# Optimization experiments

Hardware: AMD Instinct MI355X
Metric: run time of the kernel (lower is better)

The kernel has to match this reference:

```python
import jax, jax.numpy as jnp
import numpy as np

FACTOR = 1  # init factor -> top_k = int(factor * log(L))


def setup_inputs() -> dict:
    key = jax.random.key(0)
    kq, kk, kv = jax.random.split(key, 3)
    B, L, H, E = 16, 2048, 8, 64
    shape = (B, L, H, E)
    return {
        "queries": jax.random.normal(kq, shape, dtype=jnp.float32),
        "keys": jax.random.normal(kk, shape, dtype=jnp.float32),
        "values": jax.random.normal(kv, shape, dtype=jnp.float32),
    }


def reference(queries, keys, values):
    B, L, H, E = queries.shape
    # seq lens equal -> torch's pad/truncate branch is a no-op slice
    q = jnp.transpose(queries, (0, 2, 3, 1))  # [B,H,E,L]
    k = jnp.transpose(keys, (0, 2, 3, 1))
    v = jnp.transpose(values, (0, 2, 3, 1))

    # FFT-based circular cross-correlation along time
    qf = jnp.fft.rfft(q, axis=-1)
    kf = jnp.fft.rfft(k, axis=-1)
    corr = jnp.fft.irfft(qf * jnp.conj(kf), n=L, axis=-1)  # [B,H,E,L]

    top_k = int(FACTOR * np.log(L))  # static: 7 for L=2048
    mean_value = corr.mean(axis=(1, 2))  # mean over head then variates -> [B,L]
    # global (batch-averaged) top-k delays, shared across batch (training path)
    _, topk_index = jax.lax.top_k(mean_value.mean(axis=0), top_k)  # [k]
    # per-batch weights at those delays, softmax over k
    w = jax.nn.softmax(mean_value[:, topk_index], axis=-1)  # [B,k]

    # torch.roll(v, -d, -1)[..., t] == v[..., (t + d) % L]
    idx = (jnp.arange(L)[None, :] + topk_index[:, None]) % L  # [k,L]
    gathered = v[..., idx]  # [B,H,E,k,L]
    agg = jnp.einsum('bhekl,bk->bhel', gathered, w)  # weighted delay aggregation

    return jnp.transpose(agg, (0, 3, 1, 2))  # back to [B,L,H,E]
```

## Files before the change

kernel.cpp:

```cpp
#include <hip/hip_runtime.h>
#include <hip/hip_bf16.h>
#include <hip/hip_fp16.h>
#include <math.h>


#define B_ 16
#define L_ 2048
#define H_ 8
#define E_ 64
#define K_ 7
#define RS_ 2178

#define Z_OFF    0ull
#define PART_OFF 67108864ull
#define MV_OFF   (PART_OFF + 16777216ull)
#define TK_OFF   (MV_OFF + 131072ull)
#define W_OFF    (TK_OFF + 64ull)

__device__ __forceinline__ float2 cadd(float2 a, float2 b) { return make_float2(a.x + b.x, a.y + b.y); }
__device__ __forceinline__ float2 csub(float2 a, float2 b) { return make_float2(a.x - b.x, a.y - b.y); }
__device__ __forceinline__ float2 cmul(float2 a, float2 b) {
  return make_float2(fmaf(a.x, b.x, -a.y * b.y), fmaf(a.x, b.y, a.y * b.x));
}
__device__ __forceinline__ float2 cis(float ang) { float s, c; sincosf(ang, &s, &c); return make_float2(c, s); }

template<int S> __device__ __forceinline__ float2 rot90(float2 z) {
  return (S < 0) ? make_float2(z.y, -z.x) : make_float2(-z.y, z.x);
}
template<int S> __device__ __forceinline__ void dft4(float2& a, float2& b, float2& c, float2& d) {
  float2 t0 = cadd(a, c), t1 = csub(a, c), t2 = cadd(b, d), t3 = rot90<S>(csub(b, d));
  a = cadd(t0, t2); c = csub(t0, t2); b = cadd(t1, t3); d = csub(t1, t3);
}
template<int S> __device__ __forceinline__ void dft8(float2 v[8]) {
  const float RT = 0.70710678118654752f;
  const float SR = (S < 0) ? -RT : RT;
  float2 a0 = cadd(v[0], v[4]), a1 = cadd(v[1], v[5]), a2 = cadd(v[2], v[6]), a3 = cadd(v[3], v[7]);
  float2 b0 = csub(v[0], v[4]), b1 = csub(v[1], v[5]), b2 = csub(v[2], v[6]), b3 = csub(v[3], v[7]);
  b1 = cmul(b1, make_float2(RT, SR));
  b2 = rot90<S>(b2);
  b3 = cmul(b3, make_float2(-RT, SR));
  dft4<S>(a0, a1, a2, a3);
  dft4<S>(b0, b1, b2, b3);
  v[0] = a0; v[2] = a1; v[4] = a2; v[6] = a3;
  v[1] = b0; v[3] = b1; v[5] = b2; v[7] = b3;
}
__device__ __forceinline__ int sg(int e) { return e + (e >> 4); }

__device__ __forceinline__ float2 ld16(const __half2* p) { return __half22float2(*p); }
__device__ __forceinline__ void st16(__half2* p, float2 v) { *p = __float22half2_rn(v); }

__global__ __launch_bounds__(512) void pack_kernel(
    const float* __restrict__ q, const float* __restrict__ k,
    float4* __restrict__ z) {
  extern __shared__ float4 tile[];
  int tid = threadIdx.x;
  int l = blockIdx.x;
  int tl = l & 63, b = l >> 6;
  size_t rowbase = ((size_t)b * L_ + tl * 32) * 512;
  const float4* q4 = (const float4*)(q + rowbase);
  const float4* k4 = (const float4*)(k + rowbase);
#pragma unroll
  for (int pass = 0; pass < 8; ++pass) {
    int m = pass * 512 + tid;
    int j = m >> 7, cq = m & 127;
    float4 qv = q4[j * 128 + cq];
    float4 kv = k4[j * 128 + cq];
    float4 pk;
    ((__half2*)&pk)[0] = __float22half2_rn(make_float2(qv.x, kv.x));
    ((__half2*)&pk)[1] = __float22half2_rn(make_float2(qv.y, kv.y));
    ((__half2*)&pk)[2] = __float22half2_rn(make_float2(qv.z, kv.z));
    ((__half2*)&pk)[3] = __float22half2_rn(make_float2(qv.w, kv.w));
    tile[cq * 33 + j] = pk;
  }
  __syncthreads();
  float4* slab = z + (size_t)l * 4096;
#pragma unroll
  for (int pass = 0; pass < 8; ++pass) {
    int m = pass * 512 + tid;
    int cq = m >> 5, j = m & 31;
    slab[cq * 32 + j] = tile[cq * 33 + j];
  }
}

__global__ __launch_bounds__(512) void fft_corr_kernel(
    const float4* __restrict__ z, float2* __restrict__ part) {
  extern __shared__ __half2 dbuf[];
  int tid = threadIdx.x;
  int t = tid & 255;
  int half = tid >> 8;
  int j2 = t & 31, j3 = t & 3;
  int l = blockIdx.x;
  int cg = l & 63, b = l >> 6;
  int cq0 = cg * 2;
  const float4* zb = z + (size_t)b * 64 * 4096;

#pragma unroll
  for (int it = 0; it < 8; ++it) {
    int m = it * 512 + tid;
    int tl = m >> 6, inner = m & 63;
    int cqr = inner >> 5, j = inner & 31;
    float4 pk = zb[(size_t)tl * 4096 + (cq0 + cqr) * 32 + j];
    int sp = sg(tl * 32 + j);
    const __half2* hp = (const __half2*)&pk;
    dbuf[(cqr * 4 + 0) * RS_ + sp] = hp[0];
    dbuf[(cqr * 4 + 1) * RS_ + sp] = hp[1];
    dbuf[(cqr * 4 + 2) * RS_ + sp] = hp[2];
    dbuf[(cqr * 4 + 3) * RS_ + sp] = hp[3];
  }
  __syncthreads();

  float2 tw1[7], tw2[7], tw3[7];
  {
    float2 w1 = cis(-6.283185307179586f * (float)t  / 2048.0f);
    float2 w2 = cis(-6.283185307179586f * (float)j2 / 256.0f);
    float2 w3 = cis(-6.283185307179586f * (float)j3 / 32.0f);
    tw1[0] = w1; tw2[0] = w2; tw3[0] = w3;
#pragma unroll
    for (int kk = 1; kk < 7; ++kk) {
      tw1[kk] = cmul(tw1[kk - 1], w1);
      tw2[kk] = cmul(tw2[kk - 1], w2);
      tw3[kk] = cmul(tw3[kk - 1], w3);
    }
  }
  int base2 = (t >> 5) * 256 + j2;
  int base3 = (t >> 2) * 32 + j3;
  float2 acc[8];
#pragma unroll
  for (int kk = 0; kk < 8; ++kk) acc[kk] = make_float2(0.f, 0.f);

  for (int p = 0; p < 2; ++p) {
    __half2* A  = dbuf + (size_t)(4 * p + 2 * half) * RS_;
    __half2* Bf = A + RS_;
    float2 va[8], vb[8];
#pragma unroll
    for (int m = 0; m < 8; ++m) { va[m] = ld16(&A[sg(t + 256 * m)]); vb[m] = ld16(&Bf[sg(t + 256 * m)]); }
    dft8<-1>(va); dft8<-1>(vb);
#pragma unroll
    for (int kk = 1; kk < 8; ++kk) { va[kk] = cmul(va[kk], tw1[kk - 1]); vb[kk] = cmul(vb[kk], tw1[kk - 1]); }
#pragma unroll
    for (int kk = 0; kk < 8; ++kk) { st16(&A[sg(t + 256 * kk)], va[kk]); st16(&Bf[sg(t + 256 * kk)], vb[kk]); }
    __syncthreads();
#pragma unroll
    for (int m = 0; m < 8; ++m) { va[m] = ld16(&A[sg(base2 + 32 * m)]); vb[m] = ld16(&Bf[sg(base2 + 32 * m)]); }
    dft8<-1>(va); dft8<-1>(vb);
#pragma unroll
    for (int kk = 1; kk < 8; ++kk) { va[kk] = cmul(va[kk], tw2[kk - 1]); vb[kk] = cmul(vb[kk], tw2[kk - 1]); }
#pragma unroll
    for (int kk = 0; kk < 8; ++kk) { st16(&A[sg(base2 + 32 * kk)], va[kk]); st16(&Bf[sg(base2 + 32 * kk)], vb[kk]); }
    __syncthreads();
#pragma unroll
    for (int m = 0; m < 8; ++m) { va[m] = ld16(&A[sg(base3 + 4 * m)]); vb[m] = ld16(&Bf[sg(base3 + 4 * m)]); }
    dft8<-1>(va); dft8<-1>(vb);
#pragma unroll
    for (int kk = 1; kk < 8; ++kk) { va[kk] = cmul(va[kk], tw3[kk - 1]); vb[kk] = cmul(vb[kk], tw3[kk - 1]); }
#pragma unroll
    for (int kk = 0; kk < 8; ++kk) { st16(&A[sg(base3 + 4 * kk)], va[kk]); st16(&Bf[sg(base3 + 4 * kk)], vb[kk]); }
    __syncthreads();
#pragma unroll
    for (int kk = 0; kk < 8; ++kk) { va[kk] = ld16(&A[sg(8 * t + kk)]); vb[kk] = ld16(&Bf[sg(8 * t + kk)]); }
    dft4<-1>(va[0], va[1], va[2], va[3]); dft4<-1>(va[4], va[5], va[6], va[7]);
    dft4<-1>(vb[0], vb[1], vb[2], vb[3]); dft4<-1>(vb[4], vb[5], vb[6], vb[7]);
#pragma unroll
    for (int kk = 0; kk < 8; ++kk) { st16(&A[sg(8 * t + kk)], va[kk]); st16(&Bf[sg(8 * t + kk)], vb[kk]); }
    __syncthreads();
#pragma unroll
    for (int kk = 0; kk < 8; ++kk) {
      int pos = 8 * t + kk;
      int f  = ((pos >> 8) & 7) | (((pos >> 5) & 7) << 3) | (((pos >> 2) & 7) << 6) | ((pos & 3) << 9);
      int fp = (2048 - f) & 2047;
      int pp = ((fp & 7) << 8) | (((fp >> 3) & 7) << 5) | (((fp >> 6) & 7) << 2) | ((fp >> 9) & 3);
      float2 Ax = va[kk], Bc = ld16(&A[sg(pp)]);
      acc[kk].x += 0.5f  * (Bc.x * Ax.y + Bc.y * Ax.x);
      acc[kk].y += 0.25f * (Ax.x * Ax.x + Ax.y * Ax.y - Bc.x * Bc.x - Bc.y * Bc.y);
      Ax = vb[kk]; Bc = ld16(&Bf[sg(pp)]);
      acc[kk].x += 0.5f  * (Bc.x * Ax.y + Bc.y * Ax.x);
      acc[kk].y += 0.25f * (Ax.x * Ax.x + Ax.y * Ax.y - Bc.x * Bc.x - Bc.y * Bc.y);
    }
  }
  {
    float* fre = (float*)dbuf + (size_t)(2 * half) * RS_;
    float* fim = fre + RS_;
#pragma unroll
    for (int kk = 0; kk < 8; ++kk) {
      int sp = sg(8 * t + kk);
      fre[sp] = acc[kk].x;
      fim[sp] = acc[kk].y;
    }
  }
  __syncthreads();
  {
    const float* r0 = (const float*)dbuf;
    const float* i0 = r0 + RS_;
    const float* r1 = r0 + 2 * RS_;
    const float* i1 = r0 + 3 * RS_;
    float2* prow = part + (size_t)l * L_;
#pragma unroll
    for (int m = 0; m < 4; ++m) {
      int p = tid + 512 * m;
      int sp = sg(p);
      prow[p] = make_float2(r0[sp] + r1[sp], i0[sp] + i1[sp]);
    }
  }
}

__global__ __launch_bounds__(256) void ifft_kernel(
    const float2* __restrict__ part, float* __restrict__ mv) {
  __shared__ float2 buf[2176];
  int t = threadIdx.x, b = blockIdx.x;
  int j2 = t & 31, j3 = t & 3;
  float2 tw1[7], tw2[7], tw3[7];
  {
    float2 w1 = cis(6.283185307179586f * (float)t  / 2048.0f);
    float2 w2 = cis(6.283185307179586f * (float)j2 / 256.0f);
    float2 w3 = cis(6.283185307179586f * (float)j3 / 32.0f);
    tw1[0] = w1; tw2[0] = w2; tw3[0] = w3;
#pragma unroll
    for (int kk = 1; kk < 7; ++kk) {
      tw1[kk] = cmul(tw1[kk - 1], w1);
      tw2[kk] = cmul(tw2[kk - 1], w2);
      tw3[kk] = cmul(tw3[kk - 1], w3);
    }
  }
  int base2 = (t >> 5) * 256 + j2;
  int base3 = (t >> 2) * 32 + j3;
  float2 u[8];
#pragma unroll
  for (int kk = 0; kk < 8; ++kk) u[kk] = make_float2(0.f, 0.f);
#pragma unroll 4
  for (int g = 0; g < 64; ++g) {
    const float4* rp = (const float4*)(part + (size_t)(b * 64 + g) * L_);
#pragma unroll
    for (int m = 0; m < 4; ++m) {
      float4 f = rp[4 * t + m];
      u[2 * m].x     += f.x; u[2 * m].y     += f.y;
      u[2 * m + 1].x += f.z; u[2 * m + 1].y += f.w;
    }
  }
  dft4<1>(u[0], u[1], u[2], u[3]);
  dft4<1>(u[4], u[5], u[6], u[7]);
#pragma unroll
  for (int kk = 0; kk < 8; ++kk) buf[sg(8 * t + kk)] = u[kk];
  __syncthreads();
  float2 v[8];
#pragma unroll
  for (int kk = 0; kk < 8; ++kk) v[kk] = buf[sg(base3 + 4 * kk)];
#pragma unroll
  for (int kk = 1; kk < 8; ++kk) v[kk] = cmul(v[kk], tw3[kk - 1]);
  dft8<1>(v);
  __syncthreads();
#pragma unroll
  for (int m = 0; m < 8; ++m) buf[sg(base3 + 4 * m)] = v[m];
  __syncthreads();
#pragma unroll
  for (int kk = 0; kk < 8; ++kk) v[kk] = buf[sg(base2 + 32 * kk)];
#pragma unroll
  for (int kk = 1; kk < 8; ++kk) v[kk] = cmul(v[kk], tw2[kk - 1]);
  dft8<1>(v);
  __syncthreads();
#pragma unroll
  for (int m = 0; m < 8; ++m) buf[sg(base2 + 32 * m)] = v[m];
  __syncthreads();
#pragma unroll
  for (int kk = 0; kk < 8; ++kk) v[kk] = buf[sg(t + 256 * kk)];
#pragma unroll
  for (int kk = 1; kk < 8; ++kk) v[kk] = cmul(v[kk], tw1[kk - 1]);
  dft8<1>(v);
  const float scale = 1.0f / (2048.0f * 512.0f);
#pragma unroll
  for (int m = 0; m < 8; ++m) mv[b * L_ + t + 256 * m] = v[m].x * scale;
}

__global__ __launch_bounds__(256) void topk_kernel(
    const float* __restrict__ mv, int* __restrict__ topk, float* __restrict__ wts) {
  __shared__ float av[2048];
  __shared__ float rv[256];
  __shared__ int   ri[256];
  __shared__ int   sidx[K_];
  int tid = threadIdx.x;
  for (int d = tid; d < 2048; d += 256) {
    float s = 0.f;
#pragma unroll
    for (int b = 0; b < B_; ++b) s += mv[b * L_ + d];
    av[d] = s;
  }
  __syncthreads();
  for (int kk = 0; kk < K_; ++kk) {
    float bv = -INFINITY; int bi = 0;
    for (int d = tid; d < 2048; d += 256) {
      float vv = av[d];
      if (vv > bv) { bv = vv; bi = d; }
    }
    rv[tid] = bv; ri[tid] = bi;
    __syncthreads();
    for (int off = 128; off > 0; off >>= 1) {
      if (tid < off) {
        float v2 = rv[tid + off]; int i2 = ri[tid + off];
        if (v2 > rv[tid] || (v2 == rv[tid] && i2 < ri[tid])) { rv[tid] = v2; ri[tid] = i2; }
      }
      __syncthreads();
    }
    if (tid == 0) { sidx[kk] = ri[0]; av[ri[0]] = -INFINITY; }
    __syncthreads();
  }
  if (tid < K_) topk[tid] = sidx[tid];
  if (tid < B_) {
    float xk[K_], m = -INFINITY;
#pragma unroll
    for (int kk = 0; kk < K_; ++kk) { xk[kk] = mv[tid * L_ + sidx[kk]]; m = fmaxf(m, xk[kk]); }
    float s = 0.f;
#pragma unroll
    for (int kk = 0; kk < K_; ++kk) { xk[kk] = expf(xk[kk] - m); s += xk[kk]; }
#pragma unroll
    for (int kk = 0; kk < K_; ++kk) wts[tid * K_ + kk] = xk[kk] / s;
  }
}

__global__ __launch_bounds__(256) void aggregate_kernel(
    const float4* __restrict__ v4, const int* __restrict__ topk,
    const float* __restrict__ wts, float4* __restrict__ out4) {
  __shared__ int   sidx[K_];
  __shared__ float sw[B_][K_];
  int tid = threadIdx.x;
  if (tid < K_) sidx[tid] = topk[tid];
  if (tid < B_ * K_) sw[tid / K_][tid % K_] = wts[tid];
  __syncthreads();
  int idx = blockIdx.x * 256 + tid;
  int c4  = idx & 127;
  int row = idx >> 7;
  int t   = row & (L_ - 1);
  int b   = row >> 11;
  float4 acc = make_float4(0.f, 0.f, 0.f, 0.f);
#pragma unroll
  for (int kk = 0; kk < K_; ++kk) {
    int s = t + sidx[kk];
    if (s >= L_) s -= L_;
    float w = sw[b][kk];
    float4 val = v4[((size_t)(b * L_ + s) << 7) + c4];
    acc.x += w * val.x; acc.y += w * val.y;
    acc.z += w * val.z; acc.w += w * val.w;
  }
  out4[idx] = acc;
}

extern "C" void kernel_launch(void* const* d_in, const int* in_sizes, int n_in,
                              void* d_out, int out_size, void* d_ws, size_t ws_size,
                              hipStream_t stream) {
  const float* q = (const float*)d_in[0];
  const float* k = (const float*)d_in[1];
  const float* v = (const float*)d_in[2];
  float* out = (float*)d_out;

  char* ws = (char*)d_ws;
  float4* z    = (float4*)(ws + Z_OFF);
  float2* part = (float2*)(ws + PART_OFF);
  float*  mv   = (float*) (ws + MV_OFF);
  int*    topk = (int*)   (ws + TK_OFF);
  float*  wts  = (float*) (ws + W_OFF);

  pack_kernel<<<B_ * 64, 512, 4224 * sizeof(float4), stream>>>(q, k, z);
  fft_corr_kernel<<<B_ * 64, 512, 8 * RS_ * 4, stream>>>(z, part);
  ifft_kernel<<<B_, 256, 0, stream>>>(part, mv);
  topk_kernel<<<1, 256, 0, stream>>>(mv, topk, wts);
  aggregate_kernel<<<(B_ * L_ * H_ * E_ / 4) / 256, 256, 0, stream>>>(
      (const float4*)v, topk, wts, (float4*)out);
}
```

Before: 183.0 us.

## Run forward FFT in packed half2 arithmetic and split cross-block reduction into separate kernel

The forward FFT butterflies now run in packed half2 arithmetic: two channels share one __half2 lane pair, and the twiddles are stored as half2. The pack kernel reorders its halves to match. Each block now handles one channel-quad with 256 threads instead of two quads with 512, so twice as many blocks launch and each stores a larger part buffer. A new reduce kernel sums the 128 partial spectra per batch in parallel, replacing the serial 64-row loop in the single-block-per-batch ifft kernel. Doing the butterflies and twiddles in fp16 loses precision compared with the earlier fp16-storage, fp32-compute scheme.

```diff
diff --git a/kernel.cpp b/kernel.cpp
--- a/kernel.cpp
+++ b/kernel.cpp
@@ -13,7 +13,8 @@
 
 #define Z_OFF    0ull
 #define PART_OFF 67108864ull
-#define MV_OFF   (PART_OFF + 16777216ull)
+#define S_OFF    (PART_OFF + 33554432ull)
+#define MV_OFF   (S_OFF + 262144ull)
 #define TK_OFF   (MV_OFF + 131072ull)
 #define W_OFF    (TK_OFF + 64ull)
 
@@ -46,8 +47,40 @@
 }
 __device__ __forceinline__ int sg(int e) { return e + (e >> 4); }
 
-__device__ __forceinline__ float2 ld16(const __half2* p) { return __half22float2(*p); }
-__device__ __forceinline__ void st16(__half2* p, float2 v) { *p = __float22half2_rn(v); }
+struct hc { __half2 re, im; };
+__device__ __forceinline__ hc hcadd(hc a, hc b) { return { __hadd2(a.re, b.re), __hadd2(a.im, b.im) }; }
+__device__ __forceinline__ hc hcsub(hc a, hc b) { return { __hsub2(a.re, b.re), __hsub2(a.im, b.im) }; }
+template<int S> __device__ __forceinline__ hc hrot90(hc z) {
+  hc r; if (S < 0) { r.re = z.im; r.im = __hneg2(z.re); } else { r.re = __hneg2(z.im); r.im = z.re; }
+  return r;
+}
+__device__ __forceinline__ hc hcmul(hc v, __half2 wre, __half2 wim) {
+  hc r;
+  r.re = __hsub2(__hmul2(v.re, wre), __hmul2(v.im, wim));
+  r.im = __hfma2(v.re, wim, __hmul2(v.im, wre));
+  return r;
+}
+template<int S> __device__ __forceinline__ void hdft4(hc& a, hc& b, hc& c, hc& d) {
+  hc t0 = hcadd(a, c), t1 = hcsub(a, c), t2 = hcadd(b, d), t3 = hrot90<S>(hcsub(b, d));
+  a = hcadd(t0, t2); c = hcsub(t0, t2); b = hcadd(t1, t3); d = hcsub(t1, t3);
+}
+template<int S> __device__ __forceinline__ void hdft8(hc v[8]) {
+  const float RT = 0.70710678118654752f;
+  __half2 rt  = __float2half2_rn(RT);
+  __half2 sr  = __float2half2_rn((S < 0) ? -RT : RT);
+  __half2 nrt = __float2half2_rn(-RT);
+  hc a0 = hcadd(v[0], v[4]), a1 = hcadd(v[1], v[5]), a2 = hcadd(v[2], v[6]), a3 = hcadd(v[3], v[7]);
+  hc b0 = hcsub(v[0], v[4]), b1 = hcsub(v[1], v[5]), b2 = hcsub(v[2], v[6]), b3 = hcsub(v[3], v[7]);
+  b1 = hcmul(b1, rt, sr);
+  b2 = hrot90<S>(b2);
+  b3 = hcmul(b3, nrt, sr);
+  hdft4<S>(a0, a1, a2, a3);
+  hdft4<S>(b0, b1, b2, b3);
+  v[0] = a0; v[2] = a1; v[4] = a2; v[6] = a3;
+  v[1] = b0; v[3] = b1; v[5] = b2; v[7] = b3;
+}
+__device__ __forceinline__ __half2 u2h(unsigned u) { return __builtin_bit_cast(__half2, u); }
+__device__ __forceinline__ unsigned h2u(__half2 h) { return __builtin_bit_cast(unsigned, h); }
 
 __global__ __launch_bounds__(512) void pack_kernel(
     const float* __restrict__ q, const float* __restrict__ k,
@@ -66,10 +99,10 @@
     float4 qv = q4[j * 128 + cq];
     float4 kv = k4[j * 128 + cq];
     float4 pk;
-    ((__half2*)&pk)[0] = __float22half2_rn(make_float2(qv.x, kv.x));
-    ((__half2*)&pk)[1] = __float22half2_rn(make_float2(qv.y, kv.y));
-    ((__half2*)&pk)[2] = __float22half2_rn(make_float2(qv.z, kv.z));
-    ((__half2*)&pk)[3] = __float22half2_rn(make_float2(qv.w, kv.w));
+    ((__half2*)&pk)[0] = __float22half2_rn(make_float2(qv.x, qv.y));
+    ((__half2*)&pk)[1] = __float22half2_rn(make_float2(kv.x, kv.y));
+    ((__half2*)&pk)[2] = __float22half2_rn(make_float2(qv.z, qv.w));
+    ((__half2*)&pk)[3] = __float22half2_rn(make_float2(kv.z, kv.w));
     tile[cq * 33 + j] = pk;
   }
   __syncthreads();
@@ -82,44 +115,37 @@
   }
 }
 
-__global__ __launch_bounds__(512) void fft_corr_kernel(
+__global__ __launch_bounds__(256) void fft_corr_kernel(
     const float4* __restrict__ z, float2* __restrict__ part) {
-  extern __shared__ __half2 dbuf[];
-  int tid = threadIdx.x;
-  int t = tid & 255;
-  int half = tid >> 8;
+  extern __shared__ uint2 dbuf[];
+  int t = threadIdx.x;
   int j2 = t & 31, j3 = t & 3;
   int l = blockIdx.x;
-  int cg = l & 63, b = l >> 6;
-  int cq0 = cg * 2;
+  int cg = l & 127, b = l >> 7;
   const float4* zb = z + (size_t)b * 64 * 4096;
 
 #pragma unroll
   for (int it = 0; it < 8; ++it) {
-    int m = it * 512 + tid;
-    int tl = m >> 6, inner = m & 63;
-    int cqr = inner >> 5, j = inner & 31;
-    float4 pk = zb[(size_t)tl * 4096 + (cq0 + cqr) * 32 + j];
+    int m = it * 256 + t;
+    int tl = m >> 5, j = m & 31;
+    float4 pk = zb[(size_t)tl * 4096 + cg * 32 + j];
     int sp = sg(tl * 32 + j);
-    const __half2* hp = (const __half2*)&pk;
-    dbuf[(cqr * 4 + 0) * RS_ + sp] = hp[0];
-    dbuf[(cqr * 4 + 1) * RS_ + sp] = hp[1];
-    dbuf[(cqr * 4 + 2) * RS_ + sp] = hp[2];
-    dbuf[(cqr * 4 + 3) * RS_ + sp] = hp[3];
-  }
-  __syncthreads();
-
-  float2 tw1[7], tw2[7], tw3[7];
+    dbuf[sp]       = make_uint2(__float_as_uint(pk.x), __float_as_uint(pk.y));
+    dbuf[RS_ + sp] = make_uint2(__float_as_uint(pk.z), __float_as_uint(pk.w));
+  }
+
+  __half2 t1re[7], t1im[7], t2re[7], t2im[7], t3re[7], t3im[7];
   {
     float2 w1 = cis(-6.283185307179586f * (float)t  / 2048.0f);
     float2 w2 = cis(-6.283185307179586f * (float)j2 / 256.0f);
     float2 w3 = cis(-6.283185307179586f * (float)j3 / 32.0f);
-    tw1[0] = w1; tw2[0] = w2; tw3[0] = w3;
-#pragma unroll
-    for (int kk = 1; kk < 7; ++kk) {
-      tw1[kk] = cmul(tw1[kk - 1], w1);
-      tw2[kk] = cmul(tw2[kk - 1], w2);
-      tw3[kk] = cmul(tw3[kk - 1], w3);
+    float2 a1 = w1, a2 = w2, a3 = w3;
+#pragma unroll
+    for (int kk = 0; kk < 7; ++kk) {
+      t1re[kk] = __float2half2_rn(a1.x); t1im[kk] = __float2half2_rn(a1.y);
+      t2re[kk] = __float2half2_rn(a2.x); t2im[kk] = __float2half2_rn(a2.y);
+      t3re[kk] = __float2half2_rn(a3.x); t3im[kk] = __float2half2_rn(a3.y);
+      a1 = cmul(a1, w1); a2 = cmul(a2, w2); a3 = cmul(a3, w3);
     }
   }
   int base2 = (t >> 5) * 256 + j2;
@@ -127,41 +153,40 @@
   float2 acc[8];
 #pragma unroll
   for (int kk = 0; kk < 8; ++kk) acc[kk] = make_float2(0.f, 0.f);
+  __syncthreads();
 
   for (int p = 0; p < 2; ++p) {
-    __half2* A  = dbuf + (size_t)(4 * p + 2 * half) * RS_;
-    __half2* Bf = A + RS_;
-    float2 va[8], vb[8];
-#pragma unroll
-    for (int m = 0; m < 8; ++m) { va[m] = ld16(&A[sg(t + 256 * m)]); vb[m] = ld16(&Bf[sg(t + 256 * m)]); }
-    dft8<-1>(va); dft8<-1>(vb);
-#pragma unroll
-    for (int kk = 1; kk < 8; ++kk) { va[kk] = cmul(va[kk], tw1[kk - 1]); vb[kk] = cmul(vb[kk], tw1[kk - 1]); }
-#pragma unroll
-    for (int kk = 0; kk < 8; ++kk) { st16(&A[sg(t + 256 * kk)], va[kk]); st16(&Bf[sg(t + 256 * kk)], vb[kk]); }
-    __syncthreads();
-#pragma unroll
-    for (int m = 0; m < 8; ++m) { va[m] = ld16(&A[sg(base2 + 32 * m)]); vb[m] = ld16(&Bf[sg(base2 + 32 * m)]); }
-    dft8<-1>(va); dft8<-1>(vb);
-#pragma unroll
-    for (int kk = 1; kk < 8; ++kk) { va[kk] = cmul(va[kk], tw2[kk - 1]); vb[kk] = cmul(vb[kk], tw2[kk - 1]); }
-#pragma unroll
-    for (int kk = 0; kk < 8; ++kk) { st16(&A[sg(base2 + 32 * kk)], va[kk]); st16(&Bf[sg(base2 + 32 * kk)], vb[kk]); }
-    __syncthreads();
-#pragma unroll
-    for (int m = 0; m < 8; ++m) { va[m] = ld16(&A[sg(base3 + 4 * m)]); vb[m] = ld16(&Bf[sg(base3 + 4 * m)]); }
-    dft8<-1>(va); dft8<-1>(vb);
-#pragma unroll
-    for (int kk = 1; kk < 8; ++kk) { va[kk] = cmul(va[kk], tw3[kk - 1]); vb[kk] = cmul(vb[kk], tw3[kk - 1]); }
-#pragma unroll
-    for (int kk = 0; kk < 8; ++kk) { st16(&A[sg(base3 + 4 * kk)], va[kk]); st16(&Bf[sg(base3 + 4 * kk)], vb[kk]); }
-    __syncthreads();
-#pragma unroll
-    for (int kk = 0; kk < 8; ++kk) { va[kk] = ld16(&A[sg(8 * t + kk)]); vb[kk] = ld16(&Bf[sg(8 * t + kk)]); }
-    dft4<-1>(va[0], va[1], va[2], va[3]); dft4<-1>(va[4], va[5], va[6], va[7]);
-    dft4<-1>(vb[0], vb[1], vb[2], vb[3]); dft4<-1>(vb[4], vb[5], vb[6], vb[7]);
-#pragma unroll
-    for (int kk = 0; kk < 8; ++kk) { st16(&A[sg(8 * t + kk)], va[kk]); st16(&Bf[sg(8 * t + kk)], vb[kk]); }
+    uint2* R = dbuf + (size_t)p * RS_;
+    hc v[8];
+#pragma unroll
+    for (int m = 0; m < 8; ++m) { uint2 u = R[sg(t + 256 * m)]; v[m].re = u2h(u.x); v[m].im = u2h(u.y); }
+    hdft8<-1>(v);
+#pragma unroll
+    for (int kk = 1; kk < 8; ++kk) v[kk] = hcmul(v[kk], t1re[kk - 1], t1im[kk - 1]);
+#pragma unroll
+    for (int kk = 0; kk < 8; ++kk) R[sg(t + 256 * kk)] = make_uint2(h2u(v[kk].re), h2u(v[kk].im));
+    __syncthreads();
+#pragma unroll
+    for (int m = 0; m < 8; ++m) { uint2 u = R[sg(base2 + 32 * m)]; v[m].re = u2h(u.x); v[m].im = u2h(u.y); }
+    hdft8<-1>(v);
+#pragma unroll
+    for (int kk = 1; kk < 8; ++kk) v[kk] = hcmul(v[kk], t2re[kk - 1], t2im[kk - 1]);
+#pragma unroll
+    for (int kk = 0; kk < 8; ++kk) R[sg(base2 + 32 * kk)] = make_uint2(h2u(v[kk].re), h2u(v[kk].im));
+    __syncthreads();
+#pragma unroll
+    for (int m = 0; m < 8; ++m) { uint2 u = R[sg(base3 + 4 * m)]; v[m].re = u2h(u.x); v[m].im = u2h(u.y); }
+    hdft8<-1>(v);
+#pragma unroll
+    for (int kk = 1; kk < 8; ++kk) v[kk] = hcmul(v[kk], t3re[kk - 1], t3im[kk - 1]);
+#pragma unroll
+    for (int kk = 0; kk < 8; ++kk) R[sg(base3 + 4 * kk)] = make_uint2(h2u(v[kk].re), h2u(v[kk].im));
+    __syncthreads();
+#pragma unroll
+    for (int kk = 0; kk < 8; ++kk) { uint2 u = R[sg(8 * t + kk)]; v[kk].re = u2h(u.x); v[kk].im = u2h(u.y); }
+    hdft4<-1>(v[0], v[1], v[2], v[3]); hdft4<-1>(v[4], v[5], v[6], v[7]);
+#pragma unroll
+    for (int kk = 0; kk < 8; ++kk) R[sg(8 * t + kk)] = make_uint2(h2u(v[kk].re), h2u(v[kk].im));
     __syncthreads();
 #pragma unroll
     for (int kk = 0; kk < 8; ++kk) {
@@ -169,42 +194,50 @@
       int f  = ((pos >> 8) & 7) | (((pos >> 5) & 7) << 3) | (((pos >> 2) & 7) << 6) | ((pos & 3) << 9);
       int fp = (2048 - f) & 2047;
       int pp = ((fp & 7) << 8) | (((fp >> 3) & 7) << 5) | (((fp >> 6) & 7) << 2) | ((fp >> 9) & 3);
-      float2 Ax = va[kk], Bc = ld16(&A[sg(pp)]);
-      acc[kk].x += 0.5f  * (Bc.x * Ax.y + Bc.y * Ax.x);
-      acc[kk].y += 0.25f * (Ax.x * Ax.x + Ax.y * Ax.y - Bc.x * Bc.x - Bc.y * Bc.y);
-      Ax = vb[kk]; Bc = ld16(&Bf[sg(pp)]);
-      acc[kk].x += 0.5f  * (Bc.x * Ax.y + Bc.y * Ax.x);
-      acc[kk].y += 0.25f * (Ax.x * Ax.x + Ax.y * Ax.y - Bc.x * Bc.x - Bc.y * Bc.y);
-    }
-  }
-  {
-    float* fre = (float*)dbuf + (size_t)(2 * half) * RS_;
-    float* fim = fre + RS_;
-#pragma unroll
-    for (int kk = 0; kk < 8; ++kk) {
-      int sp = sg(8 * t + kk);
-      fre[sp] = acc[kk].x;
-      fim[sp] = acc[kk].y;
-    }
-  }
-  __syncthreads();
-  {
-    const float* r0 = (const float*)dbuf;
-    const float* i0 = r0 + RS_;
-    const float* r1 = r0 + 2 * RS_;
-    const float* i1 = r0 + 3 * RS_;
+      uint2 ub = R[sg(pp)];
+      __half2 bre = u2h(ub.x), bim = u2h(ub.y);
+      float ar0 = __low2float(v[kk].re),  ar1 = __high2float(v[kk].re);
+      float ai0 = __low2float(v[kk].im),  ai1 = __high2float(v[kk].im);
+      float br0 = __low2float(bre),       br1 = __high2float(bre);
+      float bi0 = __low2float(bim),       bi1 = __high2float(bim);
+      acc[kk].x += 0.5f  * ((br0 * ai0 + bi0 * ar0) + (br1 * ai1 + bi1 * ar1));
+      acc[kk].y += 0.25f * ((ar0 * ar0 + ai0 * ai0 - br0 * br0 - bi0 * bi0)
+                          + (ar1 * ar1 + ai1 * ai1 - br1 * br1 - bi1 * bi1));
+    }
+  }
+  {
+    float2* pk0 = (float2*)dbuf;
+#pragma unroll
+    for (int kk = 0; kk < 8; ++kk) pk0[sg(8 * t + kk)] = acc[kk];
+  }
+  __syncthreads();
+  {
+    const float2* pk0 = (const float2*)dbuf;
     float2* prow = part + (size_t)l * L_;
 #pragma unroll
-    for (int m = 0; m < 4; ++m) {
-      int p = tid + 512 * m;
-      int sp = sg(p);
-      prow[p] = make_float2(r0[sp] + r1[sp], i0[sp] + i1[sp]);
-    }
-  }
+    for (int m = 0; m < 8; ++m) {
+      int p = t + 256 * m;
+      prow[p] = pk0[sg(p)];
+    }
+  }
+}
+
+__global__ __launch_bounds__(256) void reduce_S_kernel(
+    const float2* __restrict__ part, float2* __restrict__ S) {
+  int idx = blockIdx.x * 256 + threadIdx.x;
+  int p = idx & 2047;
+  int b = idx >> 11;
+  float2 s = make_float2(0.f, 0.f);
+#pragma unroll 4
+  for (int i = 0; i < 128; ++i) {
+    float2 vv = part[(size_t)(b * 128 + i) * L_ + p];
+    s.x += vv.x; s.y += vv.y;
+  }
+  S[idx] = s;
 }
 
 __global__ __launch_bounds__(256) void ifft_kernel(
-    const float2* __restrict__ part, float* __restrict__ mv) {
+    const float2* __restrict__ S, float* __restrict__ mv) {
   __shared__ float2 buf[2176];
   int t = threadIdx.x, b = blockIdx.x;
   int j2 = t & 31, j3 = t & 3;
@@ -224,16 +257,13 @@
   int base2 = (t >> 5) * 256 + j2;
   int base3 = (t >> 2) * 32 + j3;
   float2 u[8];
-#pragma unroll
-  for (int kk = 0; kk < 8; ++kk) u[kk] = make_float2(0.f, 0.f);
-#pragma unroll 4
-  for (int g = 0; g < 64; ++g) {
-    const float4* rp = (const float4*)(part + (size_t)(b * 64 + g) * L_);
+  {
+    const float4* rp = (const float4*)(S + (size_t)b * L_);
 #pragma unroll
     for (int m = 0; m < 4; ++m) {
       float4 f = rp[4 * t + m];
-      u[2 * m].x     += f.x; u[2 * m].y     += f.y;
-      u[2 * m + 1].x += f.z; u[2 * m + 1].y += f.w;
+      u[2 * m]     = make_float2(f.x, f.y);
+      u[2 * m + 1] = make_float2(f.z, f.w);
     }
   }
   dft4<1>(u[0], u[1], u[2], u[3]);
@@ -353,13 +383,15 @@
   char* ws = (char*)d_ws;
   float4* z    = (float4*)(ws + Z_OFF);
   float2* part = (float2*)(ws + PART_OFF);
+  float2* S    = (float2*)(ws + S_OFF);
   float*  mv   = (float*) (ws + MV_OFF);
   int*    topk = (int*)   (ws + TK_OFF);
   float*  wts  = (float*) (ws + W_OFF);
 
   pack_kernel<<<B_ * 64, 512, 4224 * sizeof(float4), stream>>>(q, k, z);
-  fft_corr_kernel<<<B_ * 64, 512, 8 * RS_ * 4, stream>>>(z, part);
-  ifft_kernel<<<B_, 256, 0, stream>>>(part, mv);
+  fft_corr_kernel<<<B_ * 128, 256, 2 * RS_ * sizeof(uint2), stream>>>(z, part);
+  reduce_S_kernel<<<(B_ * L_) / 256, 256, 0, stream>>>(part, S);
+  ifft_kernel<<<B_, 256, 0, stream>>>(S, mv);
   topk_kernel<<<1, 256, 0, stream>>>(mv, topk, wts);
   aggregate_kernel<<<(B_ * L_ * H_ * E_ / 4) / 256, 256, 0, stream>>>(
       (const float4*)v, topk, wts, (float4*)out);
```

Result: faster. 159.8 us (-12.7%).
